# Kernel tuning notes

Hardware: AMD Instinct MI355X
Metric: run time of the kernel (lower is better)

Reference implementation:

```python
import jax, jax.numpy as jnp
import numpy as np
import math

DIM = 1024
MLP = 4096
D_STATE = 16
D_CONV = 4
EXPAND = 2
D_INNER = EXPAND * DIM
HALF = D_INNER // 2
DT_RANK = math.ceil(DIM / 16)
BSZ = 2
SEQ = 2048
LN_EPS = 1e-5


def setup_inputs() -> dict:
    key = jax.random.key(0)
    ks = jax.random.split(key, 12)
    s = lambda k, shape, sc: jax.random.normal(k, shape, dtype=jnp.float32) * sc
    return {
        "x": s(ks[0], (BSZ, SEQ, DIM), 1.0),
        "ln1_g": jnp.ones((DIM,), jnp.float32),
        "ln1_b": jnp.zeros((DIM,), jnp.float32),
        "in_proj_w": s(ks[1], (D_INNER, DIM), 0.02),
        "conv_x_w": s(ks[2], (HALF, 1, D_CONV), 0.1),
        "conv_x_b": jnp.zeros((HALF,), jnp.float32),
        "conv_z_w": s(ks[3], (HALF, 1, D_CONV), 0.1),
        "conv_z_b": jnp.zeros((HALF,), jnp.float32),
        "x_proj_w": s(ks[4], (DT_RANK + 2 * D_STATE, HALF), 0.02),
        "dt_proj_w": s(ks[5], (HALF, DT_RANK), 0.02),
        "dt_proj_b": s(ks[6], (HALF,), 0.1),
        "A_log": jnp.log(jnp.tile(jnp.arange(1, D_STATE + 1, dtype=jnp.float32), (HALF, 1))),
        "Dp": jnp.ones((HALF,), jnp.float32),
        "out_proj_w": s(ks[7], (DIM, D_INNER), 0.02),
        "ln2_g": jnp.ones((DIM,), jnp.float32),
        "ln2_b": jnp.zeros((DIM,), jnp.float32),
        "mlp_w1": s(ks[8], (MLP, DIM), 0.02),
        "mlp_b1": jnp.zeros((MLP,), jnp.float32),
        "mlp_w2": s(ks[9], (DIM, MLP), 0.02),
        "mlp_b2": jnp.zeros((DIM,), jnp.float32),
    }


def _ln(x, g, b):
    mu = jnp.mean(x, -1, keepdims=True)
    v = jnp.mean((x - mu) ** 2, -1, keepdims=True)
    return (x - mu) * jax.lax.rsqrt(v + LN_EPS) * g + b


def _dwconv_same(x, w, b):
    # x: [B, C, L]; w: [C, 1, K] depthwise; PyTorch 'same' pads left=(K-1)//2, right=rest
    total = D_CONV - 1
    left = total // 2
    y = jax.lax.conv_general_dilated(
        x, w, (1,), [(left, total - left)],
        dimension_numbers=("NCH", "OIH", "NCH"),
        feature_group_count=x.shape[1])
    return y + b[None, :, None]


def _mixer(x, in_proj_w, conv_x_w, conv_x_b, conv_z_w, conv_z_b,
           x_proj_w, dt_proj_w, dt_proj_b, A_log, Dp, out_proj_w):
    Bsz = x.shape[0]
    xz = jnp.einsum('bld,ed->ble', x, in_proj_w)              # [B,L,2*HALF]
    xs, zs = jnp.split(xz, 2, axis=-1)
    xc = jax.nn.silu(_dwconv_same(jnp.swapaxes(xs, 1, 2), conv_x_w, conv_x_b))  # [B,HALF,L]
    zc = jax.nn.silu(_dwconv_same(jnp.swapaxes(zs, 1, 2), conv_z_w, conv_z_b))  # [B,HALF,L]
    u = jnp.swapaxes(xc, 1, 2)                                 # [B,L,HALF]
    x_dbl = jnp.einsum('bld,ed->ble', u, x_proj_w)             # [B,L,dt_rank+2N]
    dt, Bm, Cm = jnp.split(x_dbl, [DT_RANK, DT_RANK + D_STATE], axis=-1)
    delta = jax.nn.softplus(jnp.einsum('blr,dr->bld', dt, dt_proj_w) + dt_proj_b)  # [B,L,HALF]
    A = -jnp.exp(A_log)                                        # [HALF,N]
    dA = jnp.exp(jnp.einsum('bld,dn->lbdn', delta, A))         # [L,B,HALF,N]
    dBu = jnp.einsum('bld,bln,bld->lbdn', delta, Bm, u)        # [L,B,HALF,N]
    Cs = jnp.moveaxis(Cm, 1, 0)                                # [L,B,N]

    def step(h, t):
        dA_t, dBu_t, c_t = t
        h = dA_t * h + dBu_t                                   # [B,HALF,N]
        return h, jnp.einsum('bdn,bn->bd', h, c_t)

    h0 = jnp.zeros((Bsz, HALF, D_STATE), x.dtype)
    _, ys = jax.lax.scan(step, h0, (dA, dBu, Cs))              # ys: [L,B,HALF]
    y = jnp.moveaxis(ys, 0, 1) + u * Dp                        # [B,L,HALF]
    y = jnp.concatenate([y, jnp.swapaxes(zc, 1, 2)], axis=-1)  # [B,L,2*HALF]
    return jnp.einsum('ble,de->bld', y, out_proj_w)


def reference(x, ln1_g, ln1_b, in_proj_w, conv_x_w, conv_x_b, conv_z_w, conv_z_b,
              x_proj_w, dt_proj_w, dt_proj_b, A_log, Dp, out_proj_w,
              ln2_g, ln2_b, mlp_w1, mlp_b1, mlp_w2, mlp_b2):
    x = x + _mixer(_ln(x, ln1_g, ln1_b), in_proj_w, conv_x_w, conv_x_b,
                   conv_z_w, conv_z_b, x_proj_w, dt_proj_w, dt_proj_b,
                   A_log, Dp, out_proj_w)
    h = _ln(x, ln2_g, ln2_b)
    h = jax.nn.gelu(jnp.einsum('bld,md->blm', h, mlp_w1) + mlp_b1, approximate=False)
    h = jnp.einsum('blm,dm->bld', h, mlp_w2) + mlp_b2
    return x + h
```

## Files before the change

### kernel.cpp

```cpp
#include <hip/hip_runtime.h>
#include <math.h>

#define DIMD    1024
#define MLPD    4096
#define DSTATE  16
#define DCONV   4
#define HALF    1024
#define DINNER  2048
#define DTRANK  64
#define BSZ     2
#define SEQ     2048
#define NTOK    (BSZ*SEQ)
#define NCH     64
#define CL      (SEQ/NCH)

typedef short bf16x8 __attribute__((ext_vector_type(8)));
typedef float f32x4  __attribute__((ext_vector_type(4)));
typedef float f32x16 __attribute__((ext_vector_type(16)));
typedef unsigned short u16;
typedef unsigned int   u32;
typedef unsigned short u16x4 __attribute__((ext_vector_type(4)));

__device__ __forceinline__ u16 f2bf(float x) {
    union { float f; unsigned int u; } v; v.f = x;
    unsigned int r = (v.u + 0x7FFFu + ((v.u >> 16) & 1u)) >> 16;
    return (u16)r;
}
__device__ __forceinline__ float bf2f(u16 x) {
    union { unsigned int u; float f; } v; v.u = ((unsigned int)x) << 16;
    return v.f;
}

#define SZ_WIN  (DINNER*DIMD)
#define SZ_WXP  (96*HALF)
#define SZ_WDT  (HALF*DTRANK)
#define SZ_WOUT (DIMD*DINNER)
#define SZ_WM1  (MLPD*DIMD)
#define SZ_WM2  (DIMD*MLPD)
#define SZ_TOT  (SZ_WIN+SZ_WXP+SZ_WDT+SZ_WOUT+SZ_WM1+SZ_WM2)
#define CVT_BLOCKS (SZ_TOT / 1024)

__global__ __launch_bounds__(256) void cvtln_kernel(
        const float* __restrict__ x, const float* __restrict__ g,
        const float* __restrict__ b, u16* __restrict__ xn_bf,
        const float* __restrict__ s0, u16* __restrict__ d0,
        const float* __restrict__ s1, u16* __restrict__ d1,
        const float* __restrict__ s2, u16* __restrict__ d2,
        const float* __restrict__ s3, u16* __restrict__ d3,
        const float* __restrict__ s4, u16* __restrict__ d4,
        const float* __restrict__ s5, u16* __restrict__ d5) {
    if (blockIdx.x >= NTOK) {
        int i = (blockIdx.x - NTOK) * 1024 + threadIdx.x * 4;
        #define CVT4(s, d) { \
            float4 v = *(const float4*)((s) + i); \
            u16x4 o; o[0]=f2bf(v.x); o[1]=f2bf(v.y); o[2]=f2bf(v.z); o[3]=f2bf(v.w); \
            *(u16x4*)((d) + i) = o; }
        if (i < SZ_WIN)  { CVT4(s0, d0); return; }  i -= SZ_WIN;
        if (i < SZ_WXP)  { CVT4(s1, d1); return; }  i -= SZ_WXP;
        if (i < SZ_WDT)  { CVT4(s2, d2); return; }  i -= SZ_WDT;
        if (i < SZ_WOUT) { CVT4(s3, d3); return; }  i -= SZ_WOUT;
        if (i < SZ_WM1)  { CVT4(s4, d4); return; }  i -= SZ_WM1;
        if (i < SZ_WM2)  { CVT4(s5, d5); }
        #undef CVT4
        return;
    }
    __shared__ float sm[4];
    int row = blockIdx.x;
    int t = threadIdx.x;
    const float4* xr = (const float4*)(x + (size_t)row * DIMD);
    float4 v = xr[t];
    float s = v.x + v.y + v.z + v.w;
    for (int off = 32; off > 0; off >>= 1) s += __shfl_down(s, off, 64);
    if ((t & 63) == 0) sm[t >> 6] = s;
    __syncthreads();
    float mu = (sm[0] + sm[1] + sm[2] + sm[3]) * (1.0f / DIMD);
    float dx = v.x - mu, dy = v.y - mu, dz = v.z - mu, dw = v.w - mu;
    float ss = dx*dx + dy*dy + dz*dz + dw*dw;
    for (int off = 32; off > 0; off >>= 1) ss += __shfl_down(ss, off, 64);
    __syncthreads();
    if ((t & 63) == 0) sm[t >> 6] = ss;
    __syncthreads();
    float var = (sm[0] + sm[1] + sm[2] + sm[3]) * (1.0f / DIMD);
    float rs = rsqrtf(var + 1e-5f);
    float4 gv = ((const float4*)g)[t];
    float4 bv = ((const float4*)b)[t];
    u16* o = xn_bf + (size_t)row * DIMD + t * 4;
    o[0] = f2bf(dx * rs * gv.x + bv.x);
    o[1] = f2bf(dy * rs * gv.y + bv.y);
    o[2] = f2bf(dz * rs * gv.z + bv.z);
    o[3] = f2bf(dw * rs * gv.w + bv.w);
}

__global__ __launch_bounds__(256) void gemm_small_kernel(
        const u16* __restrict__ A, int lda,
        const u16* __restrict__ W, int K, int N,
        float* __restrict__ Cf, u16* __restrict__ Cb) {
    __shared__ f32x4 red[2][64];
    int t = threadIdx.x;
    int w = t >> 6, lane = t & 63;
    int mt = w & 1, kh = w >> 1;
    int m0 = blockIdx.x * 32 + mt * 16;
    int n0 = blockIdx.y * 16;
    int r = lane & 15, quad = lane >> 4;
    int Kh = K >> 1;
    f32x4 acc = {0.f, 0.f, 0.f, 0.f};
    const u16* ap = A + (size_t)(m0 + r) * lda + kh * Kh + quad * 8;
    const u16* wp = W + (size_t)(n0 + r) * K   + kh * Kh + quad * 8;
    for (int k = 0; k < Kh; k += 32) {
        bf16x8 av = *(const bf16x8*)(ap + k);
        bf16x8 bv = *(const bf16x8*)(wp + k);
        acc = __builtin_amdgcn_mfma_f32_16x16x32_bf16(av, bv, acc, 0, 0, 0);
    }
    if (kh == 1) red[mt][lane] = acc;
    __syncthreads();
    if (kh == 0) {
        f32x4 o = red[mt][lane];
        int col = n0 + r;
        #pragma unroll
        for (int i = 0; i < 4; ++i) {
            int row = m0 + quad * 4 + i;
            size_t idx = (size_t)row * N + col;
            float v = acc[i] + o[i];
            Cf[idx] = v;
            Cb[idx] = f2bf(v);
        }
    }
}

template<int EPI, int TN, int KS>
__global__ __launch_bounds__(256) void gemm128_kernel(
        const u16* __restrict__ A, int lda, const u16* __restrict__ W,
        int K, int N,
        const float* __restrict__ bias, const float* __restrict__ resid,
        float* __restrict__ Cf, float* __restrict__ Cf2,
        float* __restrict__ Cf3, float* __restrict__ Cf4,
        u16* __restrict__ Cb) {
    constexpr int NF = TN / 32;
    constexpr int NN = TN / 64;
    __shared__ u16 As0[128 * 32], As1[128 * 32];
    __shared__ u16 Bs0[TN * 32],  Bs1[TN * 32];
    const int t = threadIdx.x;
    const int w = t >> 6;
    const int lane = t & 63;
    const int r32 = lane & 31;
    const int kh  = lane >> 5;
    const int wm = w & 1, wn = w >> 1;
    const int m0 = blockIdx.x * 128;
    const int n0 = blockIdx.y * TN;
    const int Kloc = K / KS;
    const int kz = (KS > 1) ? blockIdx.z : 0;

    f32x16 acc[2][NN];
    #pragma unroll
    for (int mi = 0; mi < 2; ++mi)
        #pragma unroll
        for (int ni = 0; ni < NN; ++ni)
            acc[mi][ni] = (f32x16){0.f,0.f,0.f,0.f,0.f,0.f,0.f,0.f,
                                   0.f,0.f,0.f,0.f,0.f,0.f,0.f,0.f};

    const u16* pa[2];
    const u16* pb[NF / 2];
    #pragma unroll
    for (int i = 0; i < 2; ++i) {
        int c = (i * 4 + w) * 64 + lane;
        int row = c >> 2;
        int q = (c & 3) ^ ((row >> 1) & 3);
        pa[i] = A + (size_t)(m0 + row) * lda + (size_t)kz * Kloc + q * 8;
    }
    #pragma unroll
    for (int i = 0; i < NF / 2; ++i) {
        int c = (i * 4 + w) * 64 + lane;
        int row = c >> 2;
        int q = (c & 3) ^ ((row >> 1) & 3);
        pb[i] = W + (size_t)(n0 + row) * K + (size_t)kz * Kloc + q * 8;
    }
    const int gsw = (r32 >> 1) & 3;
    int aoff[2][2], boff[NN][2];
    #pragma unroll
    for (int mi = 0; mi < 2; ++mi)
        #pragma unroll
        for (int tt = 0; tt < 2; ++tt)
            aoff[mi][tt] = (wm * 64 + mi * 32 + r32) * 32 +
                           ((tt * 2 + kh) ^ gsw) * 8;
    #pragma unroll
    for (int ni = 0; ni < NN; ++ni)
        #pragma unroll
        for (int tt = 0; tt < 2; ++tt)
            boff[ni][tt] = (wn * (TN / 2) + ni * 32 + r32) * 32 +
                           ((tt * 2 + kh) ^ gsw) * 8;

    auto stage = [&](u16* __restrict__ Ad, u16* __restrict__ Bd) {
        #pragma unroll
        for (int i = 0; i < 2; ++i) {
            __builtin_amdgcn_global_load_lds(
                (const __attribute__((address_space(1))) u32*)pa[i],
                (__attribute__((address_space(3))) u32*)(Ad + (i * 4 + w) * 512),
                16, 0, 0);
            pa[i] += 32;
        }
        #pragma unroll
        for (int i = 0; i < NF / 2; ++i) {
            __builtin_amdgcn_global_load_lds(
                (const __attribute__((address_space(1))) u32*)pb[i],
                (__attribute__((address_space(3))) u32*)(Bd + (i * 4 + w) * 512),
                16, 0, 0);
            pb[i] += 32;
        }
    };
    auto compute = [&](const u16* __restrict__ Ab, const u16* __restrict__ Bb) {
        bf16x8 af[2][2], bfr[NN][2];
        #pragma unroll
        for (int mi = 0; mi < 2; ++mi)
            #pragma unroll
            for (int tt = 0; tt < 2; ++tt)
                af[mi][tt] = *(const bf16x8*)(Ab + aoff[mi][tt]);
        #pragma unroll
        for (int ni = 0; ni < NN; ++ni)
            #pragma unroll
            for (int tt = 0; tt < 2; ++tt)
                bfr[ni][tt] = *(const bf16x8*)(Bb + boff[ni][tt]);
        #pragma unroll
        for (int tt = 0; tt < 2; ++tt)
            #pragma unroll
            for (int mi = 0; mi < 2; ++mi)
                #pragma unroll
                for (int ni = 0; ni < NN; ++ni)
                    acc[mi][ni] = __builtin_amdgcn_mfma_f32_32x32x16_bf16(
                        af[mi][tt], bfr[ni][tt], acc[mi][ni], 0, 0, 0);
    };

    stage(As0, Bs0);
    for (int k0 = 0; k0 < Kloc; k0 += 64) {
        __syncthreads();
        if (k0 + 32 < Kloc) stage(As1, Bs1);
        compute(As0, Bs0);
        __syncthreads();
        if (k0 + 64 < Kloc) stage(As0, Bs0);
        compute(As1, Bs1);
    }

    float* Cfo = Cf;
    if (KS == 2 && kz == 1) Cfo = Cf2;
    if (KS == 4) Cfo = (kz == 0) ? Cf : (kz == 1) ? Cf2 : (kz == 2) ? Cf3 : Cf4;
    #pragma unroll
    for (int mi = 0; mi < 2; ++mi) {
        #pragma unroll
        for (int ni = 0; ni < NN; ++ni) {
            #pragma unroll
            for (int reg = 0; reg < 16; ++reg) {
                int row = m0 + wm * 64 + mi * 32 + (reg & 3) + 8 * (reg >> 2) + 4 * kh;
                int col = n0 + wn * (TN / 2) + ni * 32 + r32;
                size_t idx = (size_t)row * N + col;
                float v = acc[mi][ni][reg];
                if (EPI == 1) { v += bias[col]; v = (v > 20.f) ? v : log1pf(expf(v)); }
                if (EPI == 2) {
                    v += bias[col];
                    float e = __expf(fminf(1.5957691216f * v + 0.0713548162f * v * v * v, 80.f));
                    v = v * __fdividef(e, e + 1.f);
                }
                if (EPI == 3) { v += resid[idx]; }
                if (EPI == 4) { v += bias[col] + resid[idx]; }
                if (EPI == 2 || EPI == 5) Cb[idx] = f2bf(v);
                else                      Cfo[idx] = v;
            }
        }
    }
}

__global__ __launch_bounds__(256) void reduce4_kernel(
        const float* __restrict__ P0, const float* __restrict__ P1,
        const float* __restrict__ P2, const float* __restrict__ P3,
        const float* __restrict__ bias, const float* __restrict__ resid,
        float* __restrict__ out) {
    size_t idx = ((size_t)blockIdx.x * 256 + threadIdx.x) * 4;
    float4 a = *(const float4*)(P0 + idx);
    float4 b = *(const float4*)(P1 + idx);
    float4 c = *(const float4*)(P2 + idx);
    float4 d = *(const float4*)(P3 + idx);
    float4 rr = *(const float4*)(resid + idx);
    int col = (int)(idx & (DIMD - 1));
    float4 bb = *(const float4*)(bias + col);
    float4 o;
    o.x = a.x + b.x + c.x + d.x + rr.x + bb.x;
    o.y = a.y + b.y + c.y + d.y + rr.y + bb.y;
    o.z = a.z + b.z + c.z + d.z + rr.z + bb.z;
    o.w = a.w + b.w + c.w + d.w + rr.w + bb.w;
    *(float4*)(out + idx) = o;
}

__global__ __launch_bounds__(256) void reduce_ln4_kernel(
        const float* __restrict__ P0, const float* __restrict__ P1,
        const float* __restrict__ P2, const float* __restrict__ P3,
        const float* __restrict__ resid,
        const float* __restrict__ g, const float* __restrict__ b,
        float* __restrict__ x2, u16* __restrict__ out_bf) {
    __shared__ float sm[4];
    int row = blockIdx.x;
    int t = threadIdx.x;
    size_t base = (size_t)row * DIMD + t * 4;
    float4 a  = *(const float4*)(P0 + base);
    float4 p  = *(const float4*)(P1 + base);
    float4 c  = *(const float4*)(P2 + base);
    float4 d  = *(const float4*)(P3 + base);
    float4 rr = *(const float4*)(resid + base);
    float4 v;
    v.x = a.x + p.x + c.x + d.x + rr.x;
    v.y = a.y + p.y + c.y + d.y + rr.y;
    v.z = a.z + p.z + c.z + d.z + rr.z;
    v.w = a.w + p.w + c.w + d.w + rr.w;
    *(float4*)(x2 + base) = v;
    float s = v.x + v.y + v.z + v.w;
    for (int off = 32; off > 0; off >>= 1) s += __shfl_down(s, off, 64);
    if ((t & 63) == 0) sm[t >> 6] = s;
    __syncthreads();
    float mu = (sm[0] + sm[1] + sm[2] + sm[3]) * (1.0f / DIMD);
    float dx = v.x - mu, dy = v.y - mu, dz = v.z - mu, dw = v.w - mu;
    float ss = dx*dx + dy*dy + dz*dz + dw*dw;
    for (int off = 32; off > 0; off >>= 1) ss += __shfl_down(ss, off, 64);
    __syncthreads();
    if ((t & 63) == 0) sm[t >> 6] = ss;
    __syncthreads();
    float var = (sm[0] + sm[1] + sm[2] + sm[3]) * (1.0f / DIMD);
    float rs = rsqrtf(var + 1e-5f);
    float4 gv = ((const float4*)g)[t];
    float4 bv = ((const float4*)b)[t];
    u16* o = out_bf + base;
    o[0] = f2bf(dx * rs * gv.x + bv.x);
    o[1] = f2bf(dy * rs * gv.y + bv.y);
    o[2] = f2bf(dz * rs * gv.z + bv.z);
    o[3] = f2bf(dw * rs * gv.w + bv.w);
}

__global__ __launch_bounds__(256) void conv_silu_kernel(
        const u16* __restrict__ xz,
        const float* __restrict__ wx, const float* __restrict__ bx,
        const float* __restrict__ wz, const float* __restrict__ bz,
        u16* __restrict__ u_bf, u16* __restrict__ ycat) {
    int c  = blockIdx.x * 256 + threadIdx.x;
    int gy = blockIdx.y;
    int b  = gy >> 8;
    int l0 = (gy & 255) * 8;
    const u16* base = xz + ((size_t)(b * SEQ + l0)) * DINNER;
    float wxr[4], wzr[4];
    #pragma unroll
    for (int k = 0; k < 4; ++k) { wxr[k] = wx[c * 4 + k]; wzr[k] = wz[c * 4 + k]; }
    float bxv = bx[c], bzv = bz[c];
    float xm1 = (l0 > 0) ? bf2f(base[c - DINNER]) : 0.f;
    float x0v = bf2f(base[c]);
    float x1v = bf2f(base[c + DINNER]);
    float zm1 = (l0 > 0) ? bf2f(base[HALF + c - DINNER]) : 0.f;
    float z0v = bf2f(base[HALF + c]);
    float z1v = bf2f(base[HALF + c + DINNER]);
    u16* up = u_bf + ((size_t)(b * SEQ + l0)) * HALF + c;
    u16* yp = ycat + ((size_t)(b * SEQ + l0)) * DINNER + HALF + c;
    #pragma unroll
    for (int l = 0; l < 8; ++l) {
        bool in = (l0 + l + 2) < SEQ;
        float x2v = in ? bf2f(base[(size_t)(l + 2) * DINNER + c]) : 0.f;
        float z2v = in ? bf2f(base[(size_t)(l + 2) * DINNER + HALF + c]) : 0.f;
        float ax = bxv + wxr[0]*xm1 + wxr[1]*x0v + wxr[2]*x1v + wxr[3]*x2v;
        float az = bzv + wzr[0]*zm1 + wzr[1]*z0v + wzr[2]*z1v + wzr[3]*z2v;
        float sx = ax * __fdividef(1.f, 1.f + __expf(-ax));
        float sz = az * __fdividef(1.f, 1.f + __expf(-az));
        *up = f2bf(sx); *yp = f2bf(sz);
        up += HALF; yp += DINNER;
        xm1 = x0v; x0v = x1v; x1v = x2v;
        zm1 = z0v; z0v = z1v; z1v = z2v;
    }
}

__global__ __launch_bounds__(256) void scan_p1_kernel(
        const float* __restrict__ delta, const u16* __restrict__ u_bf,
        const float* __restrict__ x_dbl, const float* __restrict__ A_log,
        float* __restrict__ hfin, float* __restrict__ dsum) {
    int t  = blockIdx.x * 256 + threadIdx.x;
    int d  = t & (HALF - 1);
    int ch = (t >> 10) & (NCH - 1);
    int b  = t >> 16;
    float Ac[16], h[16];
    #pragma unroll
    for (int i = 0; i < 4; ++i) {
        float4 a = *(const float4*)&A_log[d * DSTATE + i * 4];
        Ac[4*i+0] = -__expf(a.x); Ac[4*i+1] = -__expf(a.y);
        Ac[4*i+2] = -__expf(a.z); Ac[4*i+3] = -__expf(a.w);
        h[4*i+0] = 0.f; h[4*i+1] = 0.f; h[4*i+2] = 0.f; h[4*i+3] = 0.f;
    }
    int l0 = b * SEQ + ch * CL;
    size_t off = (size_t)l0 * HALF + d;
    const float* xrow = x_dbl + (size_t)l0 * 96;
    float ds = 0.f;
    #pragma unroll 4
    for (int l = 0; l < CL; ++l) {
        float dl = delta[off];
        float uv = bf2f(u_bf[off]);
        off += HALF;
        float4 B0 = *(const float4*)(xrow + 64);
        float4 B1 = *(const float4*)(xrow + 68);
        float4 B2 = *(const float4*)(xrow + 72);
        float4 B3 = *(const float4*)(xrow + 76);
        xrow += 96;
        float dBu = dl * uv;
        ds += dl;
        float Bv[16] = {B0.x,B0.y,B0.z,B0.w, B1.x,B1.y,B1.z,B1.w,
                        B2.x,B2.y,B2.z,B2.w, B3.x,B3.y,B3.z,B3.w};
        #pragma unroll
        for (int n = 0; n < 16; ++n)
            h[n] = __expf(dl * Ac[n]) * h[n] + dBu * Bv[n];
    }
    float4* hf = (float4*)&hfin[(size_t)t * 16];
    #pragma unroll
    for (int i = 0; i < 4; ++i)
        hf[i] = (float4){h[4*i+0], h[4*i+1], h[4*i+2], h[4*i+3]};
    dsum[t] = ds;
}

__global__ __launch_bounds__(256) void scan_p2_kernel(
        const float* __restrict__ A_log, const float* __restrict__ dsum,
        const float* __restrict__ hfin, float* __restrict__ hin) {
    int t = blockIdx.x * 256 + threadIdx.x;
    int n = t & 15;
    int d = (t >> 4) & (HALF - 1);
    int b = t >> 14;
    float Ac = -__expf(A_log[d * DSTATE + n]);
    float h = 0.f;
    for (int ch = 0; ch < NCH; ++ch) {
        size_t chain = ((size_t)(b * NCH + ch) * HALF) + d;
        hin[chain * 16 + n] = h;
        float ds = dsum[chain];
        h = __expf(Ac * ds) * h + hfin[chain * 16 + n];
    }
}

__global__ __launch_bounds__(256) void scan_p3_kernel(
        const float* __restrict__ delta, const u16* __restrict__ u_bf,
        const float* __restrict__ x_dbl, const float* __restrict__ A_log,
        const float* __restrict__ Dp, const float* __restrict__ hin,
        u16* __restrict__ ycat) {
    int t  = blockIdx.x * 256 + threadIdx.x;
    int d  = t & (HALF - 1);
    int ch = (t >> 10) & (NCH - 1);
    int b  = t >> 16;
    float Ac[16], h[16];
    #pragma unroll
    for (int i = 0; i < 4; ++i) {
        float4 a  = *(const float4*)&A_log[d * DSTATE + i * 4];
        float4 hv = *(const float4*)&hin[(size_t)t * 16 + i * 4];
        Ac[4*i+0] = -__expf(a.x); Ac[4*i+1] = -__expf(a.y);
        Ac[4*i+2] = -__expf(a.z); Ac[4*i+3] = -__expf(a.w);
        h[4*i+0] = hv.x; h[4*i+1] = hv.y; h[4*i+2] = hv.z; h[4*i+3] = hv.w;
    }
    float Dv = Dp[d];
    int l0 = b * SEQ + ch * CL;
    size_t off = (size_t)l0 * HALF + d;
    const float* xrow = x_dbl + (size_t)l0 * 96;
    u16* yp = ycat + (size_t)l0 * DINNER + d;
    #pragma unroll 4
    for (int l = 0; l < CL; ++l) {
        float dl = delta[off];
        float uv = bf2f(u_bf[off]);
        off += HALF;
        float4 B0 = *(const float4*)(xrow + 64);
        float4 B1 = *(const float4*)(xrow + 68);
        float4 B2 = *(const float4*)(xrow + 72);
        float4 B3 = *(const float4*)(xrow + 76);
        float4 C0 = *(const float4*)(xrow + 80);
        float4 C1 = *(const float4*)(xrow + 84);
        float4 C2 = *(const float4*)(xrow + 88);
        float4 C3 = *(const float4*)(xrow + 92);
        xrow += 96;
        float dBu = dl * uv;
        float Bv[16] = {B0.x,B0.y,B0.z,B0.w, B1.x,B1.y,B1.z,B1.w,
                        B2.x,B2.y,B2.z,B2.w, B3.x,B3.y,B3.z,B3.w};
        float Cv[16] = {C0.x,C0.y,C0.z,C0.w, C1.x,C1.y,C1.z,C1.w,
                        C2.x,C2.y,C2.z,C2.w, C3.x,C3.y,C3.z,C3.w};
        float y = uv * Dv;
        #pragma unroll
        for (int n = 0; n < 16; ++n) {
            h[n] = __expf(dl * Ac[n]) * h[n] + dBu * Bv[n];
            y += h[n] * Cv[n];
        }
        *yp = f2bf(y);
        yp += DINNER;
    }
}

extern "C" void kernel_launch(void* const* d_in, const int* in_sizes, int n_in,
                              void* d_out, int out_size, void* d_ws, size_t ws_size,
                              hipStream_t stream) {
    const float* x         = (const float*)d_in[0];
    const float* ln1_g     = (const float*)d_in[1];
    const float* ln1_b     = (const float*)d_in[2];
    const float* in_proj_w = (const float*)d_in[3];
    const float* conv_x_w  = (const float*)d_in[4];
    const float* conv_x_b  = (const float*)d_in[5];
    const float* conv_z_w  = (const float*)d_in[6];
    const float* conv_z_b  = (const float*)d_in[7];
    const float* x_proj_w  = (const float*)d_in[8];
    const float* dt_proj_w = (const float*)d_in[9];
    const float* dt_proj_b = (const float*)d_in[10];
    const float* A_log     = (const float*)d_in[11];
    const float* Dp        = (const float*)d_in[12];
    const float* out_proj_w= (const float*)d_in[13];
    const float* ln2_g     = (const float*)d_in[14];
    const float* ln2_b     = (const float*)d_in[15];
    const float* mlp_w1    = (const float*)d_in[16];
    const float* mlp_b1    = (const float*)d_in[17];
    const float* mlp_w2    = (const float*)d_in[18];
    const float* mlp_b2    = (const float*)d_in[19];
    float* out = (float*)d_out;

    char* p = (char*)d_ws;
    auto alloc = [&](size_t bytes) {
        char* r = p; p += (bytes + 255) & ~(size_t)255; return r;
    };
    const size_t MB16 = (size_t)16 * 1024 * 1024;
    u16*   w_in   = (u16*)  alloc((size_t)DINNER * DIMD * 2);
    u16*   w_xp   = (u16*)  alloc((size_t)96 * HALF * 2);
    u16*   w_dt   = (u16*)  alloc((size_t)HALF * DTRANK * 2);
    u16*   w_out  = (u16*)  alloc((size_t)DIMD * DINNER * 2);
    u16*   w_m1   = (u16*)  alloc((size_t)MLPD * DIMD * 2);
    u16*   w_m2   = (u16*)  alloc((size_t)DIMD * MLPD * 2);
    char*  Pb     =         alloc(4 * MB16);
    float* delta  = (float*)(Pb);
    u16*   xz_bf  = (u16*)  (Pb + 1 * MB16);
    u16*   ycat   = (u16*)  (Pb + 2 * MB16);
    u16*   u_bf   = (u16*)  (Pb + 3 * MB16);
    u16*   xn_bf  = (u16*)  (Pb + 3 * MB16 + MB16 / 2);
    float* x_dbl  = (float*)alloc((size_t)NTOK * 96 * 4);
    u16*   xdbl_bf= (u16*)  alloc((size_t)NTOK * 96 * 2);
    float* x2     = (float*)alloc((size_t)NTOK * DIMD * 4);
    u16*   ln2_bf = (u16*)  alloc((size_t)NTOK * DIMD * 2);
    u16*   mlp_h  = (u16*)  alloc((size_t)NTOK * MLPD * 2);
    float* hfin = (float*)mlp_h;
    float* hin  = hfin + (size_t)BSZ * NCH * HALF * DSTATE;
    float* dsum = hin  + (size_t)BSZ * NCH * HALF * DSTATE;
    float* R0 = (float*)(Pb);
    float* R1 = (float*)(Pb + 1 * MB16);
    float* R2 = (float*)mlp_h;
    float* R3 = (float*)((char*)mlp_h + MB16);
    float* Q0 = (float*)(Pb);
    float* Q1 = (float*)(Pb + 1 * MB16);
    float* Q2 = (float*)(Pb + 2 * MB16);
    float* Q3 = (float*)(Pb + 3 * MB16);

    cvtln_kernel<<<NTOK + CVT_BLOCKS, 256, 0, stream>>>(
        x, ln1_g, ln1_b, xn_bf,
        in_proj_w, w_in, x_proj_w, w_xp, dt_proj_w, w_dt,
        out_proj_w, w_out, mlp_w1, w_m1, mlp_w2, w_m2);

    gemm128_kernel<5,128,1><<<dim3(NTOK/128, DINNER/128), 256, 0, stream>>>(
        xn_bf, DIMD, w_in, DIMD, DINNER, nullptr, nullptr,
        nullptr, nullptr, nullptr, nullptr, xz_bf);

    conv_silu_kernel<<<dim3(HALF/256, NTOK/8), 256, 0, stream>>>(
        xz_bf, conv_x_w, conv_x_b, conv_z_w, conv_z_b, u_bf, ycat);

    gemm_small_kernel<<<dim3(NTOK/32, 96/16), 256, 0, stream>>>(
        u_bf, HALF, w_xp, HALF, 96, x_dbl, xdbl_bf);

    gemm128_kernel<1,64,1><<<dim3(NTOK/128, HALF/64), 256, 0, stream>>>(
        xdbl_bf, 96, w_dt, DTRANK, HALF, dt_proj_b, nullptr,
        delta, nullptr, nullptr, nullptr, nullptr);

    scan_p1_kernel<<<(BSZ*NCH*HALF)/256, 256, 0, stream>>>(
        delta, u_bf, x_dbl, A_log, hfin, dsum);
    scan_p2_kernel<<<(BSZ*HALF*DSTATE)/256, 256, 0, stream>>>(
        A_log, dsum, hfin, hin);
    scan_p3_kernel<<<(BSZ*NCH*HALF)/256, 256, 0, stream>>>(
        delta, u_bf, x_dbl, A_log, Dp, hin, ycat);

    gemm128_kernel<0,128,4><<<dim3(NTOK/128, DIMD/128, 4), 256, 0, stream>>>(
        ycat, DINNER, w_out, DINNER, DIMD, nullptr, nullptr,
        R0, R1, R2, R3, nullptr);
    reduce_ln4_kernel<<<NTOK, 256, 0, stream>>>(
        R0, R1, R2, R3, x, ln2_g, ln2_b, x2, ln2_bf);

    gemm128_kernel<2,128,1><<<dim3(NTOK/128, MLPD/128), 256, 0, stream>>>(
        ln2_bf, DIMD, w_m1, DIMD, MLPD, mlp_b1, nullptr,
        nullptr, nullptr, nullptr, nullptr, mlp_h);

    gemm128_kernel<0,128,4><<<dim3(NTOK/128, DIMD/128, 4), 256, 0, stream>>>(
        mlp_h, MLPD, w_m2, MLPD, DIMD, nullptr, nullptr,
        Q0, Q1, Q2, Q3, nullptr);
    reduce4_kernel<<<(NTOK*DIMD)/1024, 256, 0, stream>>>(
        Q0, Q1, Q2, Q3, mlp_b2, x2, out);
}
```

Baseline: 431.6 us.

## Add 256x256-tile 8-wave GEMM with phased LDS pipelining for out-proj and MLP

Adds a new GEMM kernel that uses 256x256 output tiles with 512 threads and 16x16x32 bf16 MFMA. It double-buffers operands through direct global-to-LDS loads, interleaves the loads across eight barrier-separated MFMA phases, and raises wave priority during the MFMA bursts. The out-projection, MLP up-projection (fused GELU) and MLP down-projection now use this kernel in place of the 128-tile kernel, which raises operand reuse per block. In exchange, the larger tiles halve or quarter the grid size, which risks lower occupancy and poor wave balance on the 256-CU device, and the kernel needs 128KB of LDS.

```diff
diff --git a/kernel.cpp b/kernel.cpp
--- a/kernel.cpp
+++ b/kernel.cpp
@@ -262,6 +262,141 @@
                 if (EPI == 4) { v += bias[col] + resid[idx]; }
                 if (EPI == 2 || EPI == 5) Cb[idx] = f2bf(v);
                 else                      Cfo[idx] = v;
+            }
+        }
+    }
+}
+
+template<int EPI, int KS_>
+__global__ __launch_bounds__(512) void gemm256_kernel(
+        const u16* __restrict__ A, int lda, const u16* __restrict__ W,
+        int K, int N,
+        const float* __restrict__ bias,
+        float* __restrict__ Cf, float* __restrict__ Cf2,
+        float* __restrict__ Cf3, float* __restrict__ Cf4,
+        u16* __restrict__ Cb) {
+    __shared__ u16 As[2][256 * 64];
+    __shared__ u16 Bs[2][256 * 64];
+    const int t = threadIdx.x;
+    const int lane = t & 63;
+    const int w = t >> 6;
+    const int r = lane & 15, q = lane >> 4;
+    const int wm = w >> 2, wn = w & 3;
+    const int m0 = blockIdx.x * 256;
+    const int n0 = blockIdx.y * 256;
+    const int kz = (KS_ > 1) ? blockIdx.z : 0;
+    const int Kloc = K / KS_;
+    const int NI = Kloc / 128;
+
+    f32x4 acc[8][4];
+    #pragma unroll
+    for (int mi = 0; mi < 8; ++mi)
+        #pragma unroll
+        for (int ni = 0; ni < 4; ++ni)
+            acc[mi][ni] = (f32x4){0.f, 0.f, 0.f, 0.f};
+
+    const int aoffb = (wm * 128 + r) * 64 + q * 8;
+    const int boffb = (wn * 64  + r) * 64 + q * 8;
+    const int srow = t >> 3;
+    const int scol = (t & 7) * 8;
+    const int sdst = (t >> 6) * 512;
+    const size_t kzoff = (size_t)kz * Kloc;
+
+    auto stA = [&](int buf, int T, int j) {
+        const u16* src = A + (size_t)(m0 + j * 64 + srow) * lda + kzoff + T * 64 + scol;
+        __builtin_amdgcn_global_load_lds(
+            (const __attribute__((address_space(1))) u32*)src,
+            (__attribute__((address_space(3))) u32*)(&As[buf][j * 4096 + sdst]),
+            16, 0, 0);
+    };
+    auto stB = [&](int buf, int T, int j) {
+        const u16* src = W + (size_t)(n0 + j * 64 + srow) * (size_t)K + kzoff + T * 64 + scol;
+        __builtin_amdgcn_global_load_lds(
+            (const __attribute__((address_space(1))) u32*)src,
+            (__attribute__((address_space(3))) u32*)(&Bs[buf][j * 4096 + sdst]),
+            16, 0, 0);
+    };
+
+    bf16x8 bfr[4];
+
+    #define PH(BUF, KSL, MH, STMT, VMODE)                                         \
+    do {                                                                          \
+        if (MH == 0) {                                                            \
+            _Pragma("unroll")                                                     \
+            for (int ni = 0; ni < 4; ++ni)                                        \
+                bfr[ni] = *(const bf16x8*)(&Bs[BUF][boffb + ni * 1024 + KSL * 32]); \
+        }                                                                         \
+        bf16x8 af0 = *(const bf16x8*)(&As[BUF][aoffb + (MH*4+0)*1024 + KSL*32]);  \
+        bf16x8 af1 = *(const bf16x8*)(&As[BUF][aoffb + (MH*4+1)*1024 + KSL*32]);  \
+        bf16x8 af2 = *(const bf16x8*)(&As[BUF][aoffb + (MH*4+2)*1024 + KSL*32]);  \
+        bf16x8 af3 = *(const bf16x8*)(&As[BUF][aoffb + (MH*4+3)*1024 + KSL*32]);  \
+        STMT;                                                                     \
+        VMODE;                                                                    \
+        __builtin_amdgcn_s_barrier();                                             \
+        asm volatile("s_waitcnt lgkmcnt(0)" ::: "memory");                        \
+        __builtin_amdgcn_sched_barrier(0);                                        \
+        __builtin_amdgcn_s_setprio(1);                                            \
+        _Pragma("unroll")                                                         \
+        for (int ni = 0; ni < 4; ++ni) {                                          \
+            acc[MH*4+0][ni] = __builtin_amdgcn_mfma_f32_16x16x32_bf16(af0, bfr[ni], acc[MH*4+0][ni], 0, 0, 0); \
+            acc[MH*4+1][ni] = __builtin_amdgcn_mfma_f32_16x16x32_bf16(af1, bfr[ni], acc[MH*4+1][ni], 0, 0, 0); \
+            acc[MH*4+2][ni] = __builtin_amdgcn_mfma_f32_16x16x32_bf16(af2, bfr[ni], acc[MH*4+2][ni], 0, 0, 0); \
+            acc[MH*4+3][ni] = __builtin_amdgcn_mfma_f32_16x16x32_bf16(af3, bfr[ni], acc[MH*4+3][ni], 0, 0, 0); \
+        }                                                                         \
+        __builtin_amdgcn_s_setprio(0);                                            \
+        __builtin_amdgcn_s_barrier();                                             \
+    } while (0)
+
+    #define VM_NONE do {} while (0)
+    #define VM_P3   do { if (more) asm volatile("s_waitcnt vmcnt(2)" ::: "memory"); \
+                         else      asm volatile("s_waitcnt vmcnt(0)" ::: "memory"); } while (0)
+    #define VM_P7   do { if (more) asm volatile("s_waitcnt vmcnt(2)" ::: "memory"); } while (0)
+
+    #pragma unroll
+    for (int j = 0; j < 4; ++j) stB(0, 0, j);
+    #pragma unroll
+    for (int j = 0; j < 4; ++j) stA(0, 0, j);
+    stB(1, 1, 0); stB(1, 1, 1);
+    asm volatile("s_waitcnt vmcnt(2)" ::: "memory");
+    __builtin_amdgcn_s_barrier();
+
+    for (int it = 0; it < NI; ++it) {
+        const bool more = (it + 1) < NI;
+        const int T1 = 2 * it + 1, T2 = T1 + 1, T3 = T1 + 2;
+        PH(0, 0, 0, { stB(1, T1, 2); stB(1, T1, 3); }, VM_NONE);
+        PH(0, 0, 1, { stA(1, T1, 0); stA(1, T1, 1); }, VM_NONE);
+        PH(0, 1, 0, { stA(1, T1, 2); stA(1, T1, 3); }, VM_NONE);
+        PH(0, 1, 1, { if (more) { stB(0, T2, 0); stB(0, T2, 1); } }, VM_P3);
+        PH(1, 0, 0, { if (more) { stB(0, T2, 2); stB(0, T2, 3); } }, VM_NONE);
+        PH(1, 0, 1, { if (more) { stA(0, T2, 0); stA(0, T2, 1); } }, VM_NONE);
+        PH(1, 1, 0, { if (more) { stA(0, T2, 2); stA(0, T2, 3); } }, VM_NONE);
+        PH(1, 1, 1, { if (more) { stB(1, T3, 0); stB(1, T3, 1); } }, VM_P7);
+    }
+    #undef PH
+    #undef VM_NONE
+    #undef VM_P3
+    #undef VM_P7
+
+    float* Cfo = Cf;
+    if (KS_ == 4) Cfo = (kz == 0) ? Cf : (kz == 1) ? Cf2 : (kz == 2) ? Cf3 : Cf4;
+    #pragma unroll
+    for (int mi = 0; mi < 8; ++mi) {
+        #pragma unroll
+        for (int ni = 0; ni < 4; ++ni) {
+            #pragma unroll
+            for (int i = 0; i < 4; ++i) {
+                int row = m0 + wm * 128 + mi * 16 + q * 4 + i;
+                int col = n0 + wn * 64 + ni * 16 + r;
+                size_t idx = (size_t)row * N + col;
+                float v = acc[mi][ni][i];
+                if (EPI == 2) {
+                    v += bias[col];
+                    float e = __expf(fminf(1.5957691216f * v + 0.0713548162f * v * v * v, 80.f));
+                    v = v * __fdividef(e, e + 1.f);
+                    Cb[idx] = f2bf(v);
+                } else {
+                    Cfo[idx] = v;
+                }
             }
         }
     }
@@ -569,18 +704,18 @@
     scan_p3_kernel<<<(BSZ*NCH*HALF)/256, 256, 0, stream>>>(
         delta, u_bf, x_dbl, A_log, Dp, hin, ycat);
 
-    gemm128_kernel<0,128,4><<<dim3(NTOK/128, DIMD/128, 4), 256, 0, stream>>>(
-        ycat, DINNER, w_out, DINNER, DIMD, nullptr, nullptr,
+    gemm256_kernel<0,4><<<dim3(NTOK/256, DIMD/256, 4), 512, 0, stream>>>(
+        ycat, DINNER, w_out, DINNER, DIMD, nullptr,
         R0, R1, R2, R3, nullptr);
     reduce_ln4_kernel<<<NTOK, 256, 0, stream>>>(
         R0, R1, R2, R3, x, ln2_g, ln2_b, x2, ln2_bf);
 
-    gemm128_kernel<2,128,1><<<dim3(NTOK/128, MLPD/128), 256, 0, stream>>>(
-        ln2_bf, DIMD, w_m1, DIMD, MLPD, mlp_b1, nullptr,
+    gemm256_kernel<2,1><<<dim3(NTOK/256, MLPD/256, 1), 512, 0, stream>>>(
+        ln2_bf, DIMD, w_m1, DIMD, MLPD, mlp_b1,
         nullptr, nullptr, nullptr, nullptr, mlp_h);
 
-    gemm128_kernel<0,128,4><<<dim3(NTOK/128, DIMD/128, 4), 256, 0, stream>>>(
-        mlp_h, MLPD, w_m2, MLPD, DIMD, nullptr, nullptr,
+    gemm256_kernel<0,4><<<dim3(NTOK/256, DIMD/256, 4), 512, 0, stream>>>(
+        mlp_h, MLPD, w_m2, MLPD, DIMD, nullptr,
         Q0, Q1, Q2, Q3, nullptr);
     reduce4_kernel<<<(NTOK*DIMD)/1024, 256, 0, stream>>>(
         Q0, Q1, Q2, Q3, mlp_b2, x2, out);
```

After: 435.1 us. Within noise of the previous version (+0.8%).
